# Optimization experiments

Measured on AMD Instinct MI355X. Metric: run time of the kernel, lower is better.

The kernel has to match this reference:

```python
import jax, jax.numpy as jnp
from jax import lax
import numpy as np

# dims
B, T, W, D = 8, 24, 48, 512
H = 8            # n_head
E = D // H       # head dim = 64
DI = 2 * D       # mamba d_inner (expand=2) = 1024
S = 64           # d_state
R = 32           # dt_rank = ceil(512/16)
KC = 4           # mamba depthwise conv kernel
DFF = 2048       # ffn hidden
L = T * W


def setup_inputs() -> dict:
    key = jax.random.key(0)
    ks = jax.random.split(key, 32)
    def g(i, shape, s=0.02):
        return jax.random.normal(ks[i], shape, dtype=jnp.float32) * s
    inp = {
        "x": jax.random.normal(ks[0], (B, T, W, D), dtype=jnp.float32),
        "slf_attn_mask": jnp.zeros((B, L), dtype=bool),
        # attention projections (torch Linear convention: y = x @ W.T + b)
        "Wq": g(1, (D, D)), "bq": jnp.zeros((D,), jnp.float32),
        "Wk": g(2, (D, D)), "bk": jnp.zeros((D,), jnp.float32),
        "Wv": g(3, (D, D)), "bv": jnp.zeros((D,), jnp.float32),
        "Wo": g(4, (D, D)), "bo": jnp.zeros((D,), jnp.float32),
        # mamba params
        "in_proj_w": g(5, (2 * DI, D)),
        "conv_w": g(6, (DI, KC), 0.1),
        "conv_b": jnp.zeros((DI,), jnp.float32),
        "x_proj_w": g(7, (R + 2 * S, DI)),
        "dt_proj_w": g(8, (DI, R), 0.1),
        "dt_proj_b": jnp.full((DI,), -3.0, jnp.float32),  # softplus -> small dt
        "A_log": jnp.broadcast_to(jnp.log(jnp.arange(1, S + 1, dtype=jnp.float32)), (DI, S)).copy(),
        "D_ssm": jnp.ones((DI,), jnp.float32),
        "out_proj_w": g(9, (D, DI)),
        # hybrid LayerNorm
        "ln1_g": jnp.ones((D,), jnp.float32), "ln1_b": jnp.zeros((D,), jnp.float32),
        # FFN (pre-norm)
        "ffn_w1": g(10, (DFF, D)), "ffn_b1": jnp.zeros((DFF,), jnp.float32),
        "ffn_w2": g(11, (D, DFF)), "ffn_b2": jnp.zeros((D,), jnp.float32),
        "ln2_g": jnp.ones((D,), jnp.float32), "ln2_b": jnp.zeros((D,), jnp.float32),
    }
    return inp


def _layernorm(x, g, b, eps):
    m = jnp.mean(x, -1, keepdims=True)
    v = jnp.mean(jnp.square(x - m), -1, keepdims=True)
    return (x - m) * lax.rsqrt(v + eps) * g + b


def _attention(xf, mask, Wq, bq, Wk, bk, Wv, bv, Wo, bo):
    # xf: [B, L, D]; mask: [B, L] bool (True = masked)
    b, l, _ = xf.shape
    q = (xf @ Wq.T + bq).reshape(b, l, H, E)
    k = (xf @ Wk.T + bk).reshape(b, l, H, E)
    v = (xf @ Wv.T + bv).reshape(b, l, H, E)
    scale = 1.0 / jnp.sqrt(jnp.float32(E))
    scores = jnp.einsum('blhe,bshe->bhls', q, k)                 # [B,H,L,L]
    scores = jnp.where(mask[:, None, None, :], -jnp.inf, scores)
    probs = jax.nn.softmax(scale * scores, axis=-1)
    out = jnp.einsum('bhls,bshe->blhe', probs, v).reshape(b, l, D)
    return out @ Wo.T + bo


def _mamba(xf, in_proj_w, conv_w, conv_b, x_proj_w, dt_proj_w, dt_proj_b, A_log, D_ssm, out_proj_w):
    # xf: [B, L, D]
    b, l, _ = xf.shape
    xz = xf @ in_proj_w.T                  # [B,L,2*DI]
    u, z = jnp.split(xz, 2, axis=-1)
    # causal depthwise conv1d, kernel KC
    up = jnp.pad(u, ((0, 0), (KC - 1, 0), (0, 0)))
    uc = conv_b + sum(up[:, k:k + l, :] * conv_w[:, k] for k in range(KC))
    u = jax.nn.silu(uc)                    # [B,L,DI]
    xdbc = u @ x_proj_w.T                  # [B,L,R+2S]
    dt_r, Bm, Cm = jnp.split(xdbc, [R, R + S], axis=-1)
    delta = jax.nn.softplus(dt_r @ dt_proj_w.T + dt_proj_b)   # [B,L,DI]
    A = -jnp.exp(A_log)                    # [DI,S]

    def step(h, xs):
        dt_t, u_t, B_t, C_t = xs           # [B,DI],[B,DI],[B,S],[B,S]
        dA = jnp.exp(dt_t[:, :, None] * A)                       # [B,DI,S]
        h = h * dA + (dt_t * u_t)[:, :, None] * B_t[:, None, :]
        y = jnp.einsum('bds,bs->bd', h, C_t)
        return h, y

    xs = (delta.transpose(1, 0, 2), u.transpose(1, 0, 2),
          Bm.transpose(1, 0, 2), Cm.transpose(1, 0, 2))
    h0 = jnp.zeros((b, DI, S), dtype=xf.dtype)
    _, ys = lax.scan(step, h0, xs)
    y = ys.transpose(1, 0, 2) + u * D_ssm  # [B,L,DI]
    y = y * jax.nn.silu(z)
    return y @ out_proj_w.T


def _forward(x, slf_attn_mask, Wq, bq, Wk, bk, Wv, bv, Wo, bo,
             in_proj_w, conv_w, conv_b, x_proj_w, dt_proj_w, dt_proj_b,
             A_log, D_ssm, out_proj_w, ln1_g, ln1_b,
             ffn_w1, ffn_b1, ffn_w2, ffn_b2, ln2_g, ln2_b):
    b, t, w, d = x.shape
    xf = x.reshape(b, t * w, d)
    x_attn = _attention(xf, slf_attn_mask, Wq, bq, Wk, bk, Wv, bv, Wo, bo)
    x_mamba = _mamba(xf, in_proj_w, conv_w, conv_b, x_proj_w, dt_proj_w,
                     dt_proj_b, A_log, D_ssm, out_proj_w)
    h = xf + x_attn + x_mamba
    h = _layernorm(h, ln1_g, ln1_b, 1e-5)
    # pre-norm FFN with residual
    hn = _layernorm(h, ln2_g, ln2_b, 1e-6)
    ff = jax.nn.gelu(hn @ ffn_w1.T + ffn_b1, approximate=False) @ ffn_w2.T + ffn_b2
    out = h + ff
    return out.reshape(b, t, w, d)


def reference(x, slf_attn_mask, Wq, bq, Wk, bk, Wv, bv, Wo, bo,
              in_proj_w, conv_w, conv_b, x_proj_w, dt_proj_w, dt_proj_b,
              A_log, D_ssm, out_proj_w, ln1_g, ln1_b,
              ffn_w1, ffn_b1, ffn_w2, ffn_b2, ln2_g, ln2_b):
    return _forward(x, slf_attn_mask, Wq, bq, Wk, bk, Wv, bv, Wo, bo,
                    in_proj_w, conv_w, conv_b, x_proj_w, dt_proj_w, dt_proj_b,
                    A_log, D_ssm, out_proj_w, ln1_g, ln1_b,
                    ffn_w1, ffn_b1, ffn_w2, ffn_b2, ln2_g, ln2_b)
```

## Files before the change

### kernel.cpp

```cpp
#include <hip/hip_runtime.h>
#include <hip/hip_bf16.h>
#include <math.h>

#define BB 8
#define DD 512
#define HH 8
#define EE 64
#define DI 1024
#define SS 64
#define RR 32
#define KCONV 4
#define DFF 2048
#define LL 1152
#define ML (BB*LL)
#define XS (RR + 2*SS)
#define ZSTR 2048
#define YSTR 1536

typedef short bf16x8 __attribute__((ext_vector_type(8)));
typedef float f32x4 __attribute__((ext_vector_type(4)));
typedef unsigned short u16x4 __attribute__((ext_vector_type(4)));

#define GLD_LDS(g, l) \
  __builtin_amdgcn_global_load_lds((const __attribute__((address_space(1))) void*)(g), \
                                   (__attribute__((address_space(3))) void*)(l), 16, 0, 0)

__device__ __forceinline__ float bf2f(unsigned short u) {
  return __uint_as_float(((unsigned)u) << 16);
}

template<int IMM>
__device__ __forceinline__ float swz(float x) {
  return __uint_as_float((unsigned)__builtin_amdgcn_ds_swizzle((int)__float_as_uint(x), IMM));
}

__global__ __launch_bounds__(256) void cvt_bf16(
    const float* __restrict__ s, __hip_bfloat16* __restrict__ d, int n)
{
  const int i = (blockIdx.x * 256 + threadIdx.x) * 4;
  if (i + 3 < n) {
    const float4 v = *(const float4*)(s + i);
    __hip_bfloat16 t[4] = {__float2bfloat16(v.x), __float2bfloat16(v.y),
                           __float2bfloat16(v.z), __float2bfloat16(v.w)};
    *(ushort4*)(d + i) = *(const ushort4*)t;
  } else {
    for (int k = i; k < n; ++k) d[k] = __float2bfloat16(s[k]);
  }
}

__global__ __launch_bounds__(256) void cvt_pack(
    const float* __restrict__ s, __hip_bfloat16* __restrict__ d,
    int srclen, int dststride, int dstoff, int total)
{
  const int i = blockIdx.x * 256 + threadIdx.x;
  if (i >= total) return;
  const int r = i / srclen, c = i - r * srclen;
  d[(size_t)r * dststride + dstoff + c] = __float2bfloat16(s[i]);
}

__global__ __launch_bounds__(256) void gemm_mfma(
    const __hip_bfloat16* __restrict__ A, int lda,
    const __hip_bfloat16* __restrict__ W,
    const float* __restrict__ bias,
    const float* __restrict__ res,
    void* __restrict__ Cv, void* __restrict__ Cv2,
    int M, int N, int K, int act, int mode)
{
  __shared__ __align__(16) __hip_bfloat16 As[128 * 32];
  __shared__ __align__(16) __hip_bfloat16 Ws[128 * 32];
  const int tid = threadIdx.x;
  const int wid = tid >> 6, lane = tid & 63;
  const int wr = wid >> 1, wc = wid & 1;
  const int m0 = blockIdx.y << 7, n0 = blockIdx.x << 7;
  const int r1 = tid >> 2;
  const int c1 = (tid & 3) << 3;

  const __hip_bfloat16* ga0 = A + (size_t)(m0 + r1) * lda + c1;
  const __hip_bfloat16* ga1 = A + (size_t)(m0 + 64 + r1) * lda + c1;
  const __hip_bfloat16* gw0 = W + (size_t)(n0 + r1) * K + c1;
  const __hip_bfloat16* gw1 = W + (size_t)(n0 + 64 + r1) * K + c1;
  char* lA0 = (char*)As + wid * 1024;
  char* lA1 = lA0 + 4096;
  char* lW0 = (char*)Ws + wid * 1024;
  char* lW1 = lW0 + 4096;

  f32x4 acc[4][4];
#pragma unroll
  for (int i = 0; i < 4; ++i)
#pragma unroll
    for (int j = 0; j < 4; ++j) acc[i][j] = (f32x4){0.f, 0.f, 0.f, 0.f};

  const int fm = lane & 15;
  const int q8 = (lane >> 4) << 3;

  for (int kt = 0; kt < K; kt += 32) {
    __syncthreads();
    GLD_LDS(ga0, lA0); GLD_LDS(ga1, lA1);
    GLD_LDS(gw0, lW0); GLD_LDS(gw1, lW1);
    ga0 += 32; ga1 += 32; gw0 += 32; gw1 += 32;
    __syncthreads();

    bf16x8 af[4], wf[4];
#pragma unroll
    for (int i = 0; i < 4; ++i)
      af[i] = *(const bf16x8*)((const short*)As + (wr * 64 + i * 16 + fm) * 32 + q8);
#pragma unroll
    for (int j = 0; j < 4; ++j)
      wf[j] = *(const bf16x8*)((const short*)Ws + (wc * 64 + j * 16 + fm) * 32 + q8);
#pragma unroll
    for (int i = 0; i < 4; ++i)
#pragma unroll
      for (int j = 0; j < 4; ++j)
        acc[i][j] = __builtin_amdgcn_mfma_f32_16x16x32_bf16(af[i], wf[j], acc[i][j], 0, 0, 0);
  }

  const int rquad = (lane >> 4) << 2;
#pragma unroll
  for (int j = 0; j < 4; ++j) {
    const int n = n0 + wc * 64 + j * 16 + fm;
    if (n < N) {
      const float bv = bias ? bias[n] : 0.f;
#pragma unroll
      for (int i = 0; i < 4; ++i) {
        const int mb = m0 + wr * 64 + i * 16 + rquad;
#pragma unroll
        for (int r = 0; r < 4; ++r) {
          const int m = mb + r;
          float v = acc[i][j][r] + bv;
          if (act == 1) v = 0.5f * v * (1.f + erff(v * 0.70710678118654752f));
          else if (act == 2) v = fmaxf(v, 0.f) + log1pf(expf(-fabsf(v)));
          if (mode == 3) {
            if (n < 1024) {
              ((__hip_bfloat16*)Cv)[(size_t)m * 1024 + n] = __float2bfloat16(v);
            } else {
              const int e = n - 1024;
              const int bb2 = m / LL;
              const int key = m - bb2 * LL;
              ((__hip_bfloat16*)Cv2)[((size_t)(bb2 * HH + (e >> 6)) * EE + (e & 63)) * LL + key] =
                  __float2bfloat16(v);
            }
          } else {
            const size_t off = (size_t)m * N + n;
            if (res) v += res[off];
            if (mode == 1) ((__hip_bfloat16*)Cv)[off] = __float2bfloat16(v);
            else ((float*)Cv)[off] = v;
          }
        }
      }
    }
  }
}

__global__ __launch_bounds__(256) void conv_silu(
    const __hip_bfloat16* __restrict__ xz, const float* __restrict__ cw,
    const float* __restrict__ cb, __hip_bfloat16* __restrict__ uout)
{
  const size_t idx = (size_t)blockIdx.x * 256 + threadIdx.x;
  if (idx >= (size_t)ML * DI) return;
  const int di = (int)(idx & (DI - 1));
  const int row = (int)(idx >> 10);
  const int t = row % LL;
  float acc = cb[di];
#pragma unroll
  for (int k = 0; k < KCONV; ++k) {
    if (t - (KCONV - 1) + k >= 0)
      acc = fmaf((float)xz[(size_t)(row - (KCONV - 1 - k)) * ZSTR + di],
                 cw[di * KCONV + k], acc);
  }
  uout[idx] = __float2bfloat16(acc / (1.f + __expf(-acc)));
}

#define SLOAD(P_, t0_) { _Pragma("unroll") for (int j = 0; j < 4; ++j) { \
    P_##_dt[j] = bf2f(dp[(size_t)((t0_)+j)*DI]); \
    P_##_u[j]  = bf2f(ubp[(size_t)((t0_)+j)*DI]); \
    P_##_B[j]  = *(const u16x4*)(Bp + (size_t)((t0_)+j)*XS); \
    P_##_C[j]  = *(const u16x4*)(Cp + (size_t)((t0_)+j)*XS); } }

#define SSTEP(P_, j, idx) { \
    const float dtu = P_##_dt[j] * P_##_u[j]; \
    h0 = fmaf(h0, __expf(P_##_dt[j] * Av[0]), dtu * bf2f(P_##_B[j][0])); \
    h1 = fmaf(h1, __expf(P_##_dt[j] * Av[1]), dtu * bf2f(P_##_B[j][1])); \
    h2 = fmaf(h2, __expf(P_##_dt[j] * Av[2]), dtu * bf2f(P_##_B[j][2])); \
    h3 = fmaf(h3, __expf(P_##_dt[j] * Av[3]), dtu * bf2f(P_##_B[j][3])); \
    float part = h0 * bf2f(P_##_C[j][0]); \
    part = fmaf(h1, bf2f(P_##_C[j][1]), part); \
    part = fmaf(h2, bf2f(P_##_C[j][2]), part); \
    part = fmaf(h3, bf2f(P_##_C[j][3]), part); \
    Pp[(idx)] = part; }

#define SCOMP(P_, base_) { \
    SSTEP(P_, 0, (base_)+0) SSTEP(P_, 1, (base_)+1) \
    SSTEP(P_, 2, (base_)+2) SSTEP(P_, 3, (base_)+3) }

__global__ __launch_bounds__(256) void scan_attn(
    const __hip_bfloat16* __restrict__ delta, const __hip_bfloat16* __restrict__ ubf,
    const __hip_bfloat16* __restrict__ xz, const __hip_bfloat16* __restrict__ xdbc,
    const float* __restrict__ A_log, const float* __restrict__ D_ssm,
    const __hip_bfloat16* __restrict__ qk, const __hip_bfloat16* __restrict__ vtg,
    __hip_bfloat16* __restrict__ yattn)
{
  __shared__ __align__(16) __hip_bfloat16 Qs[64][72];
  __shared__ __align__(16) __hip_bfloat16 Ks[64][72];
  __shared__ __align__(16) __hip_bfloat16 Vts[64][72];
  __shared__ __align__(16) __hip_bfloat16 Ps[4][16][72];
  const int tid = threadIdx.x;

  if (blockIdx.x < 512) {
    const int wv = (int)((blockIdx.x * 256 + tid) >> 6);
    const int lane = tid & 63;
    const int c = lane >> 4;
    const int s4 = lane & 15;
    const int g = (wv << 2) + c;
    const int b = g >> 10;
    const int di = g & (DI - 1);
    float Av[4];
#pragma unroll
    for (int kk = 0; kk < 4; ++kk)
      Av[kk] = -__expf(A_log[di * SS + (s4 << 2) + kk]);
    const float Dd = D_ssm[di];
    const size_t rb = (size_t)b * LL;
    const unsigned short* __restrict__ dp = (const unsigned short*)delta + rb * DI + di;
    const unsigned short* __restrict__ ubp = (const unsigned short*)ubf + rb * DI + di;
    const unsigned short* __restrict__ zbp = (const unsigned short*)xz + rb * ZSTR + DI + di;
    const unsigned short* __restrict__ Bp = (const unsigned short*)xdbc + rb * XS + RR + (s4 << 2);
    const unsigned short* __restrict__ Cp = Bp + SS;
    __hip_bfloat16* __restrict__ yp = yattn + rb * YSTR + di;

    float h0 = 0.f, h1 = 0.f, h2 = 0.f, h3 = 0.f;
    float Pp[16];
    float a_dt[4], a_u[4]; u16x4 a_B[4], a_C[4];
    float b_dt[4], b_u[4]; u16x4 b_B[4], b_C[4];
    float c_dt[4], c_u[4]; u16x4 c_B[4], c_C[4];
    float d_dt[4], d_u[4]; u16x4 d_B[4], d_C[4];

    float u_e = bf2f(ubp[(size_t)s4 * DI]);
    float z_e = bf2f(zbp[(size_t)s4 * ZSTR]);

    SLOAD(a, 0) SLOAD(b, 4) SLOAD(c, 8)
    for (int t0 = 0; t0 < LL; t0 += 16) {
      SLOAD(d, t0 + 12)
      SCOMP(a, 0)
      if (t0 + 16 < LL) SLOAD(a, t0 + 16)
      SCOMP(b, 4)
      float u_n = 0.f, z_n = 0.f;
      if (t0 + 16 < LL) {
        u_n = bf2f(ubp[(size_t)(t0 + 16 + s4) * DI]);
        z_n = bf2f(zbp[(size_t)(t0 + 16 + s4) * ZSTR]);
      }
      if (t0 + 20 < LL) SLOAD(b, t0 + 20)
      SCOMP(c, 8)
      if (t0 + 24 < LL) SLOAD(c, t0 + 24)
      SCOMP(d, 12)

#pragma unroll
      for (int k2 = 0; k2 < 8; ++k2) {
        const float mn = (s4 & 1) ? Pp[2*k2+1] : Pp[2*k2];
        const float ot = (s4 & 1) ? Pp[2*k2]   : Pp[2*k2+1];
        Pp[k2] = mn + swz<0x041F>(ot);
      }
#pragma unroll
      for (int k2 = 0; k2 < 4; ++k2) {
        const float mn = (s4 & 2) ? Pp[2*k2+1] : Pp[2*k2];
        const float ot = (s4 & 2) ? Pp[2*k2]   : Pp[2*k2+1];
        Pp[k2] = mn + swz<0x081F>(ot);
      }
#pragma unroll
      for (int k2 = 0; k2 < 2; ++k2) {
        const float mn = (s4 & 4) ? Pp[2*k2+1] : Pp[2*k2];
        const float ot = (s4 & 4) ? Pp[2*k2]   : Pp[2*k2+1];
        Pp[k2] = mn + swz<0x101F>(ot);
      }
      {
        const float mn = (s4 & 8) ? Pp[1] : Pp[0];
        const float ot = (s4 & 8) ? Pp[0] : Pp[1];
        Pp[0] = mn + swz<0x201F>(ot);
      }

      const float yv = (Pp[0] + u_e * Dd) * (z_e / (1.f + __expf(-z_e)));
      yp[(size_t)(t0 + s4) * YSTR] = __float2bfloat16(yv);
      u_e = u_n; z_e = z_n;
    }
    return;
  }

  const int abid = blockIdx.x - 512;
  const int w = tid >> 6, lane = tid & 63;
  const int bh = abid / (LL / 64);
  const int qtile = abid - bh * (LL / 64);
  const int b = bh >> 3, hh = bh & 7;
  const int q0 = qtile << 6;
  const size_t qbase = (size_t)b * LL * 1024 + (size_t)hh * EE;
  const size_t vtbase = (size_t)bh * EE * LL;

  const int srow = tid >> 2, sch = (tid & 3) << 4;
  {
    const __hip_bfloat16* src = qk + qbase + (size_t)(q0 + srow) * 1024 + sch;
    *(uint4*)&Qs[srow][sch]     = *(const uint4*)src;
    *(uint4*)&Qs[srow][sch + 8] = *(const uint4*)(src + 8);
  }
  __syncthreads();

  const int fm = lane & 15;
  const int q8 = (lane >> 4) << 3;
  bf16x8 af0 = *(const bf16x8*)&Qs[w * 16 + fm][q8];
  bf16x8 af1 = *(const bf16x8*)&Qs[w * 16 + fm][32 + q8];

  f32x4 oacc[4];
  float m_i[4], l_i[4];
#pragma unroll
  for (int r = 0; r < 4; ++r) { m_i[r] = -INFINITY; l_i[r] = 0.f; }
#pragma unroll
  for (int j = 0; j < 4; ++j) oacc[j] = (f32x4){0.f, 0.f, 0.f, 0.f};

  for (int kt = 0; kt < LL / 64; ++kt) {
    const int k0 = kt << 6;
    __syncthreads();
    {
      const __hip_bfloat16* ksrc = qk + qbase + 512 + (size_t)(k0 + srow) * 1024 + sch;
      const __hip_bfloat16* vsrc = vtg + vtbase + (size_t)srow * LL + k0 + sch;
      *(uint4*)&Ks[srow][sch]      = *(const uint4*)ksrc;
      *(uint4*)&Ks[srow][sch + 8]  = *(const uint4*)(ksrc + 8);
      *(uint4*)&Vts[srow][sch]     = *(const uint4*)vsrc;
      *(uint4*)&Vts[srow][sch + 8] = *(const uint4*)(vsrc + 8);
    }
    __syncthreads();

    f32x4 sacc[4];
#pragma unroll
    for (int j = 0; j < 4; ++j) sacc[j] = (f32x4){0.f, 0.f, 0.f, 0.f};
#pragma unroll
    for (int j = 0; j < 4; ++j) {
      bf16x8 kf0 = *(const bf16x8*)&Ks[j * 16 + fm][q8];
      bf16x8 kf1 = *(const bf16x8*)&Ks[j * 16 + fm][32 + q8];
      sacc[j] = __builtin_amdgcn_mfma_f32_16x16x32_bf16(af0, kf0, sacc[j], 0, 0, 0);
      sacc[j] = __builtin_amdgcn_mfma_f32_16x16x32_bf16(af1, kf1, sacc[j], 0, 0, 0);
    }

    float alpha[4];
#pragma unroll
    for (int r = 0; r < 4; ++r) {
#pragma unroll
      for (int j = 0; j < 4; ++j) sacc[j][r] *= 0.125f;
      float mt = fmaxf(fmaxf(sacc[0][r], sacc[1][r]), fmaxf(sacc[2][r], sacc[3][r]));
      mt = fmaxf(mt, swz<0x041F>(mt)); mt = fmaxf(mt, swz<0x081F>(mt));
      mt = fmaxf(mt, swz<0x101F>(mt)); mt = fmaxf(mt, swz<0x201F>(mt));
      const float mn = fmaxf(m_i[r], mt);
      alpha[r] = __expf(m_i[r] - mn);
      m_i[r] = mn;
      float p[4], rs = 0.f;
#pragma unroll
      for (int j = 0; j < 4; ++j) { p[j] = __expf(sacc[j][r] - mn); rs += p[j]; }
      rs += swz<0x041F>(rs); rs += swz<0x081F>(rs);
      rs += swz<0x101F>(rs); rs += swz<0x201F>(rs);
      l_i[r] = l_i[r] * alpha[r] + rs;
      const int qrow = ((lane >> 4) << 2) + r;
#pragma unroll
      for (int j = 0; j < 4; ++j)
        Ps[w][qrow][j * 16 + fm] = __float2bfloat16(p[j]);
    }
#pragma unroll
    for (int j = 0; j < 4; ++j)
#pragma unroll
      for (int r = 0; r < 4; ++r) oacc[j][r] *= alpha[r];

    bf16x8 pf0 = *(const bf16x8*)&Ps[w][fm][q8];
    bf16x8 pf1 = *(const bf16x8*)&Ps[w][fm][32 + q8];
#pragma unroll
    for (int j = 0; j < 4; ++j) {
      bf16x8 v0 = *(const bf16x8*)&Vts[j * 16 + fm][q8];
      bf16x8 v1 = *(const bf16x8*)&Vts[j * 16 + fm][32 + q8];
      oacc[j] = __builtin_amdgcn_mfma_f32_16x16x32_bf16(pf0, v0, oacc[j], 0, 0, 0);
      oacc[j] = __builtin_amdgcn_mfma_f32_16x16x32_bf16(pf1, v1, oacc[j], 0, 0, 0);
    }
  }

#pragma unroll
  for (int r = 0; r < 4; ++r) {
    const float inv = 1.f / l_i[r];
    const int qq = q0 + w * 16 + ((lane >> 4) << 2) + r;
#pragma unroll
    for (int j = 0; j < 4; ++j)
      yattn[((size_t)b * LL + qq) * YSTR + 1024 + hh * EE + j * 16 + fm] =
          __float2bfloat16(oacc[j][r] * inv);
  }
}

__device__ __forceinline__ float block_sum512(float val, float* sm)
{
#pragma unroll
  for (int off = 32; off; off >>= 1) val += __shfl_xor(val, off, 64);
  const int wid = threadIdx.x >> 6;
  __syncthreads();
  if ((threadIdx.x & 63) == 0) sm[wid] = val;
  __syncthreads();
  return sm[0] + sm[1] + sm[2] + sm[3];
}

__global__ __launch_bounds__(256) void ln_fused(
    const float* __restrict__ xf, const float* __restrict__ combo,
    const float* __restrict__ g1, const float* __restrict__ b1,
    const float* __restrict__ g2, const float* __restrict__ b2,
    float* __restrict__ hout, __hip_bfloat16* __restrict__ hnout)
{
  __shared__ float sm[4];
  const size_t base = (size_t)blockIdx.x * DD;
  const int t = threadIdx.x;
  const float v0 = xf[base + t] + combo[base + t];
  const float v1 = xf[base + 256 + t] + combo[base + 256 + t];
  const float mean = block_sum512(v0 + v1, sm) * (1.f / DD);
  const float d0 = v0 - mean, d1 = v1 - mean;
  const float var = block_sum512(d0 * d0 + d1 * d1, sm) * (1.f / DD);
  const float rstd = rsqrtf(var + 1e-5f);
  const float h0 = d0 * rstd * g1[t] + b1[t];
  const float h1 = d1 * rstd * g1[t + 256] + b1[t + 256];
  hout[base + t] = h0;
  hout[base + 256 + t] = h1;
  const float mean2 = block_sum512(h0 + h1, sm) * (1.f / DD);
  const float e0 = h0 - mean2, e1 = h1 - mean2;
  const float var2 = block_sum512(e0 * e0 + e1 * e1, sm) * (1.f / DD);
  const float rstd2 = rsqrtf(var2 + 1e-6f);
  hnout[base + t] = __float2bfloat16(e0 * rstd2 * g2[t] + b2[t]);
  hnout[base + 256 + t] = __float2bfloat16(e1 * rstd2 * g2[t + 256] + b2[t + 256]);
}

extern "C" void kernel_launch(void* const* d_in, const int* in_sizes, int n_in,
                              void* d_out, int out_size, void* d_ws, size_t ws_size,
                              hipStream_t stream)
{
  const float* x         = (const float*)d_in[0];
  const float* Wq        = (const float*)d_in[2];
  const float* bq        = (const float*)d_in[3];
  const float* Wk        = (const float*)d_in[4];
  const float* bk        = (const float*)d_in[5];
  const float* Wv        = (const float*)d_in[6];
  const float* bv        = (const float*)d_in[7];
  const float* Wo        = (const float*)d_in[8];
  const float* bo        = (const float*)d_in[9];
  const float* in_proj_w = (const float*)d_in[10];
  const float* conv_w    = (const float*)d_in[11];
  const float* conv_b    = (const float*)d_in[12];
  const float* x_proj_w  = (const float*)d_in[13];
  const float* dt_proj_w = (const float*)d_in[14];
  const float* dt_proj_b = (const float*)d_in[15];
  const float* A_log     = (const float*)d_in[16];
  const float* D_ssm     = (const float*)d_in[17];
  const float* out_proj_w= (const float*)d_in[18];
  const float* ln1_g     = (const float*)d_in[19];
  const float* ln1_b     = (const float*)d_in[20];
  const float* ffn_w1    = (const float*)d_in[21];
  const float* ffn_b1    = (const float*)d_in[22];
  const float* ffn_w2    = (const float*)d_in[23];
  const float* ffn_b2    = (const float*)d_in[24];
  const float* ln2_g     = (const float*)d_in[25];
  const float* ln2_b     = (const float*)d_in[26];
  float* out = (float*)d_out;

  float* ws = (float*)d_ws;
  const size_t OF_XBF = 2506752;
  const size_t OF_XZ  = OF_XBF + 2359296;
  const size_t OF_UBF = OF_XZ + 9437184;
  const size_t OF_XD  = OF_UBF + 4718592;
  const size_t OF_DF  = OF_XD + 737280;
  const size_t OF_QKV = OF_DF + 4718592;
  const size_t OF_YA  = OF_QKV + 7077888;
  const size_t OF_QB  = OF_YA + 7077888;

  __hip_bfloat16* wbf     = (__hip_bfloat16*)ws;
  __hip_bfloat16* xbf     = (__hip_bfloat16*)(ws + OF_XBF);
  __hip_bfloat16* hnbf    = (__hip_bfloat16*)(ws + OF_XBF);
  __hip_bfloat16* xz      = (__hip_bfloat16*)(ws + OF_XZ);
  __hip_bfloat16* ubf     = (__hip_bfloat16*)(ws + OF_UBF);
  float*          combo   = ws + OF_UBF;
  __hip_bfloat16* xdbc_bf = (__hip_bfloat16*)(ws + OF_XD);
  __hip_bfloat16* deltab  = (__hip_bfloat16*)(ws + OF_DF);
  __hip_bfloat16* ffbf    = (__hip_bfloat16*)(ws + OF_DF);
  __hip_bfloat16* qkbuf   = (__hip_bfloat16*)(ws + OF_QKV);
  __hip_bfloat16* vtbf    = (__hip_bfloat16*)(ws + OF_QKV + 4718592);
  __hip_bfloat16* yattn   = (__hip_bfloat16*)(ws + OF_YA);
  float*          hbuf    = ws + OF_YA;
  float*          qkvbias = ws + OF_QB;

  const size_t w_inproj = 0;
  const size_t w_xproj  = 1048576;
  const size_t w_dt     = 1310720;
  const size_t w_cat    = 1343488;
  const size_t w_q      = 2129920;
  const size_t w_f1     = 2916352;
  const size_t w_f2     = 3964928;

  const dim3 thr(256);
#define CVT(src, dst, n) cvt_bf16<<<dim3(((n)/4 + 255)/256), thr, 0, stream>>>(src, dst, n)
#define GEMM(Abf, lda_, Woff, Bptr, Rptr, Cptr, C2ptr, N_, K_, act_, md_) \
  gemm_mfma<<<dim3((N_ + 127)/128, ML/128), thr, 0, stream>>>( \
      Abf, lda_, wbf + (Woff), Bptr, Rptr, (void*)(Cptr), (void*)(C2ptr), ML, N_, K_, act_, md_)

  hipMemsetAsync((void*)(wbf + w_xproj + (size_t)160 * 1024), 0, (size_t)96 * 1024 * 2, stream);
  CVT(in_proj_w, wbf + w_inproj, 1048576);
  CVT(x_proj_w,  wbf + w_xproj,  163840);
  CVT(dt_proj_w, wbf + w_dt,     32768);
  cvt_pack<<<dim3((524288 + 255)/256), thr, 0, stream>>>(
      out_proj_w, wbf + w_cat, 1024, 1536, 0,    524288);
  cvt_pack<<<dim3((262144 + 255)/256), thr, 0, stream>>>(
      Wo,         wbf + w_cat, 512,  1536, 1024, 262144);
  CVT(Wq,        wbf + w_q,           262144);
  CVT(Wk,        wbf + w_q + 262144,  262144);
  CVT(Wv,        wbf + w_q + 524288,  262144);
  CVT(ffn_w1,    wbf + w_f1,    1048576);
  CVT(ffn_w2,    wbf + w_f2,    1048576);
  CVT(x,         xbf,           ML * DD);
  hipMemcpyAsync(qkvbias,        bq, 512 * sizeof(float), hipMemcpyDeviceToDevice, stream);
  hipMemcpyAsync(qkvbias + 512,  bk, 512 * sizeof(float), hipMemcpyDeviceToDevice, stream);
  hipMemcpyAsync(qkvbias + 1024, bv, 512 * sizeof(float), hipMemcpyDeviceToDevice, stream);

  GEMM(xbf, DD, w_inproj, nullptr, nullptr, xz, nullptr, 2 * DI, DD, 0, 1);
  conv_silu<<<dim3((ML * DI) / 256), thr, 0, stream>>>(xz, conv_w, conv_b, ubf);
  GEMM(ubf, DI, w_xproj, nullptr, nullptr, xdbc_bf, nullptr, XS, DI, 0, 1);
  GEMM(xdbc_bf, XS, w_dt, dt_proj_b, nullptr, deltab, nullptr, DI, RR, 2, 1);

  GEMM(xbf, DD, w_q, qkvbias, nullptr, qkbuf, vtbf, 3 * DD, DD, 0, 3);

  scan_attn<<<dim3(512 + BB * HH * (LL / 64)), thr, 0, stream>>>(
      deltab, ubf, xz, xdbc_bf, A_log, D_ssm, qkbuf, vtbf, yattn);

  GEMM(yattn, YSTR, w_cat, bo, nullptr, combo, nullptr, DD, YSTR, 0, 0);

  ln_fused<<<dim3(ML), thr, 0, stream>>>(x, combo, ln1_g, ln1_b,
                                         ln2_g, ln2_b, hbuf, hnbf);

  GEMM(hnbf, DD, w_f1, ffn_b1, nullptr, ffbf, nullptr, DFF, DD, 1, 1);
  GEMM(ffbf, DFF, w_f2, ffn_b2, hbuf, out, nullptr, DD, DFF, 0, 0);
#undef GEMM
#undef CVT
}
```

Baseline: 1.036 ms.

## Split fused scan/attention kernel and spread SSM state across full wavefront

Splits the combined scan+attention kernel into two separate launches, one for attention and one for the selective scan. The scan now gives each wavefront one (batch, channel) pair with one state element per lane (64 lanes), where before each lane handled 4 states. This cuts per-thread serial work and registers, which allows 8 blocks per CU and 4x more scan waves. It also precomputes dt*u at load time and uses exp2f with a log2e-scaled A. In exchange the kernels no longer overlap within a single launch, and each step needs a longer cross-lane reduction (extra swizzle and shuffle), with redundant B/C/dt loads per lane.

```diff
diff --git a/kernel.cpp b/kernel.cpp
--- a/kernel.cpp
+++ b/kernel.cpp
@@ -19,7 +19,6 @@
 
 typedef short bf16x8 __attribute__((ext_vector_type(8)));
 typedef float f32x4 __attribute__((ext_vector_type(4)));
-typedef unsigned short u16x4 __attribute__((ext_vector_type(4)));
 
 #define GLD_LDS(g, l) \
   __builtin_amdgcn_global_load_lds((const __attribute__((address_space(1))) void*)(g), \
@@ -171,124 +170,112 @@
 }
 
 #define SLOAD(P_, t0_) { _Pragma("unroll") for (int j = 0; j < 4; ++j) { \
-    P_##_dt[j] = bf2f(dp[(size_t)((t0_)+j)*DI]); \
-    P_##_u[j]  = bf2f(ubp[(size_t)((t0_)+j)*DI]); \
-    P_##_B[j]  = *(const u16x4*)(Bp + (size_t)((t0_)+j)*XS); \
-    P_##_C[j]  = *(const u16x4*)(Cp + (size_t)((t0_)+j)*XS); } }
+    const float dtv = bf2f(dp[(size_t)((t0_)+j)*DI]); \
+    P_##_dt[j] = dtv; \
+    P_##_du[j] = dtv * bf2f(ubp[(size_t)((t0_)+j)*DI]); \
+    P_##_B[j]  = Bp[(size_t)((t0_)+j)*XS]; \
+    P_##_C[j]  = Cp[(size_t)((t0_)+j)*XS]; } }
 
 #define SSTEP(P_, j, idx) { \
-    const float dtu = P_##_dt[j] * P_##_u[j]; \
-    h0 = fmaf(h0, __expf(P_##_dt[j] * Av[0]), dtu * bf2f(P_##_B[j][0])); \
-    h1 = fmaf(h1, __expf(P_##_dt[j] * Av[1]), dtu * bf2f(P_##_B[j][1])); \
-    h2 = fmaf(h2, __expf(P_##_dt[j] * Av[2]), dtu * bf2f(P_##_B[j][2])); \
-    h3 = fmaf(h3, __expf(P_##_dt[j] * Av[3]), dtu * bf2f(P_##_B[j][3])); \
-    float part = h0 * bf2f(P_##_C[j][0]); \
-    part = fmaf(h1, bf2f(P_##_C[j][1]), part); \
-    part = fmaf(h2, bf2f(P_##_C[j][2]), part); \
-    part = fmaf(h3, bf2f(P_##_C[j][3]), part); \
-    Pp[(idx)] = part; }
+    const float dA = exp2f(P_##_dt[j] * Av); \
+    h = fmaf(h, dA, P_##_du[j] * bf2f(P_##_B[j])); \
+    Pp[(idx)] = h * bf2f(P_##_C[j]); }
 
 #define SCOMP(P_, base_) { \
     SSTEP(P_, 0, (base_)+0) SSTEP(P_, 1, (base_)+1) \
     SSTEP(P_, 2, (base_)+2) SSTEP(P_, 3, (base_)+3) }
 
-__global__ __launch_bounds__(256) void scan_attn(
+__global__ __launch_bounds__(256, 8) void scan_kernel(
     const __hip_bfloat16* __restrict__ delta, const __hip_bfloat16* __restrict__ ubf,
     const __hip_bfloat16* __restrict__ xz, const __hip_bfloat16* __restrict__ xdbc,
     const float* __restrict__ A_log, const float* __restrict__ D_ssm,
-    const __hip_bfloat16* __restrict__ qk, const __hip_bfloat16* __restrict__ vtg,
     __hip_bfloat16* __restrict__ yattn)
+{
+  const int wv = (int)((blockIdx.x * 256 + threadIdx.x) >> 6);
+  const int lane = threadIdx.x & 63;
+  const int b = wv >> 10;
+  const int di = wv & (DI - 1);
+  const float Av = -__expf(A_log[di * SS + lane]) * 1.4426950408889634f;
+  const float Dd = D_ssm[di];
+  const size_t rb = (size_t)b * LL;
+  const unsigned short* __restrict__ dp  = (const unsigned short*)delta + rb * DI + di;
+  const unsigned short* __restrict__ ubp = (const unsigned short*)ubf + rb * DI + di;
+  const unsigned short* __restrict__ zbp = (const unsigned short*)xz + rb * ZSTR + DI + di;
+  const unsigned short* __restrict__ Bp  = (const unsigned short*)xdbc + rb * XS + RR + lane;
+  const unsigned short* __restrict__ Cp  = Bp + SS;
+  __hip_bfloat16* __restrict__ yp = yattn + rb * YSTR + di;
+
+  const int l15 = lane & 15;
+  float h = 0.f;
+  float Pp[16];
+  float a_dt[4], a_du[4]; unsigned short a_B[4], a_C[4];
+  float b_dt[4], b_du[4]; unsigned short b_B[4], b_C[4];
+
+  float u_e = bf2f(ubp[(size_t)l15 * DI]);
+  float z_e = bf2f(zbp[(size_t)l15 * ZSTR]);
+
+  SLOAD(a, 0)
+  for (int t0 = 0; t0 < LL; t0 += 16) {
+    SLOAD(b, t0 + 4)
+    SCOMP(a, 0)
+    SLOAD(a, t0 + 8)
+    SCOMP(b, 4)
+    float u_n = 0.f, z_n = 0.f;
+    if (t0 + 16 < LL) {
+      u_n = bf2f(ubp[(size_t)(t0 + 16 + l15) * DI]);
+      z_n = bf2f(zbp[(size_t)(t0 + 16 + l15) * ZSTR]);
+    }
+    SLOAD(b, t0 + 12)
+    SCOMP(a, 8)
+    if (t0 + 16 < LL) SLOAD(a, t0 + 16)
+    SCOMP(b, 12)
+
+#pragma unroll
+    for (int k2 = 0; k2 < 8; ++k2) {
+      const float mn = (lane & 1) ? Pp[2*k2+1] : Pp[2*k2];
+      const float ot = (lane & 1) ? Pp[2*k2]   : Pp[2*k2+1];
+      Pp[k2] = mn + swz<0x041F>(ot);
+    }
+#pragma unroll
+    for (int k2 = 0; k2 < 4; ++k2) {
+      const float mn = (lane & 2) ? Pp[2*k2+1] : Pp[2*k2];
+      const float ot = (lane & 2) ? Pp[2*k2]   : Pp[2*k2+1];
+      Pp[k2] = mn + swz<0x081F>(ot);
+    }
+#pragma unroll
+    for (int k2 = 0; k2 < 2; ++k2) {
+      const float mn = (lane & 4) ? Pp[2*k2+1] : Pp[2*k2];
+      const float ot = (lane & 4) ? Pp[2*k2]   : Pp[2*k2+1];
+      Pp[k2] = mn + swz<0x101F>(ot);
+    }
+    {
+      const float mn = (lane & 8) ? Pp[1] : Pp[0];
+      const float ot = (lane & 8) ? Pp[0] : Pp[1];
+      Pp[0] = mn + swz<0x201F>(ot);
+    }
+    Pp[0] += swz<0x401F>(Pp[0]);
+    Pp[0] += __shfl_xor(Pp[0], 32, 64);
+
+    const float yv = (Pp[0] + u_e * Dd) * (z_e / (1.f + __expf(-z_e)));
+    if (lane < 16)
+      yp[(size_t)(t0 + lane) * YSTR] = __float2bfloat16(yv);
+    u_e = u_n; z_e = z_n;
+  }
+}
+
+__global__ __launch_bounds__(256) void attn_mfma(
+    const __hip_bfloat16* __restrict__ qk,
+    const __hip_bfloat16* __restrict__ vtg, __hip_bfloat16* __restrict__ yattn)
 {
   __shared__ __align__(16) __hip_bfloat16 Qs[64][72];
   __shared__ __align__(16) __hip_bfloat16 Ks[64][72];
   __shared__ __align__(16) __hip_bfloat16 Vts[64][72];
   __shared__ __align__(16) __hip_bfloat16 Ps[4][16][72];
   const int tid = threadIdx.x;
-
-  if (blockIdx.x < 512) {
-    const int wv = (int)((blockIdx.x * 256 + tid) >> 6);
-    const int lane = tid & 63;
-    const int c = lane >> 4;
-    const int s4 = lane & 15;
-    const int g = (wv << 2) + c;
-    const int b = g >> 10;
-    const int di = g & (DI - 1);
-    float Av[4];
-#pragma unroll
-    for (int kk = 0; kk < 4; ++kk)
-      Av[kk] = -__expf(A_log[di * SS + (s4 << 2) + kk]);
-    const float Dd = D_ssm[di];
-    const size_t rb = (size_t)b * LL;
-    const unsigned short* __restrict__ dp = (const unsigned short*)delta + rb * DI + di;
-    const unsigned short* __restrict__ ubp = (const unsigned short*)ubf + rb * DI + di;
-    const unsigned short* __restrict__ zbp = (const unsigned short*)xz + rb * ZSTR + DI + di;
-    const unsigned short* __restrict__ Bp = (const unsigned short*)xdbc + rb * XS + RR + (s4 << 2);
-    const unsigned short* __restrict__ Cp = Bp + SS;
-    __hip_bfloat16* __restrict__ yp = yattn + rb * YSTR + di;
-
-    float h0 = 0.f, h1 = 0.f, h2 = 0.f, h3 = 0.f;
-    float Pp[16];
-    float a_dt[4], a_u[4]; u16x4 a_B[4], a_C[4];
-    float b_dt[4], b_u[4]; u16x4 b_B[4], b_C[4];
-    float c_dt[4], c_u[4]; u16x4 c_B[4], c_C[4];
-    float d_dt[4], d_u[4]; u16x4 d_B[4], d_C[4];
-
-    float u_e = bf2f(ubp[(size_t)s4 * DI]);
-    float z_e = bf2f(zbp[(size_t)s4 * ZSTR]);
-
-    SLOAD(a, 0) SLOAD(b, 4) SLOAD(c, 8)
-    for (int t0 = 0; t0 < LL; t0 += 16) {
-      SLOAD(d, t0 + 12)
-      SCOMP(a, 0)
-      if (t0 + 16 < LL) SLOAD(a, t0 + 16)
-      SCOMP(b, 4)
-      float u_n = 0.f, z_n = 0.f;
-      if (t0 + 16 < LL) {
-        u_n = bf2f(ubp[(size_t)(t0 + 16 + s4) * DI]);
-        z_n = bf2f(zbp[(size_t)(t0 + 16 + s4) * ZSTR]);
-      }
-      if (t0 + 20 < LL) SLOAD(b, t0 + 20)
-      SCOMP(c, 8)
-      if (t0 + 24 < LL) SLOAD(c, t0 + 24)
-      SCOMP(d, 12)
-
-#pragma unroll
-      for (int k2 = 0; k2 < 8; ++k2) {
-        const float mn = (s4 & 1) ? Pp[2*k2+1] : Pp[2*k2];
-        const float ot = (s4 & 1) ? Pp[2*k2]   : Pp[2*k2+1];
-        Pp[k2] = mn + swz<0x041F>(ot);
-      }
-#pragma unroll
-      for (int k2 = 0; k2 < 4; ++k2) {
-        const float mn = (s4 & 2) ? Pp[2*k2+1] : Pp[2*k2];
-        const float ot = (s4 & 2) ? Pp[2*k2]   : Pp[2*k2+1];
-        Pp[k2] = mn + swz<0x081F>(ot);
-      }
-#pragma unroll
-      for (int k2 = 0; k2 < 2; ++k2) {
-        const float mn = (s4 & 4) ? Pp[2*k2+1] : Pp[2*k2];
-        const float ot = (s4 & 4) ? Pp[2*k2]   : Pp[2*k2+1];
-        Pp[k2] = mn + swz<0x101F>(ot);
-      }
-      {
-        const float mn = (s4 & 8) ? Pp[1] : Pp[0];
-        const float ot = (s4 & 8) ? Pp[0] : Pp[1];
-        Pp[0] = mn + swz<0x201F>(ot);
-      }
-
-      const float yv = (Pp[0] + u_e * Dd) * (z_e / (1.f + __expf(-z_e)));
-      yp[(size_t)(t0 + s4) * YSTR] = __float2bfloat16(yv);
-      u_e = u_n; z_e = z_n;
-    }
-    return;
-  }
-
-  const int abid = blockIdx.x - 512;
   const int w = tid >> 6, lane = tid & 63;
-  const int bh = abid / (LL / 64);
-  const int qtile = abid - bh * (LL / 64);
+  const int bh = blockIdx.y;
   const int b = bh >> 3, hh = bh & 7;
-  const int q0 = qtile << 6;
+  const int q0 = blockIdx.x << 6;
   const size_t qbase = (size_t)b * LL * 1024 + (size_t)hh * EE;
   const size_t vtbase = (size_t)bh * EE * LL;
 
@@ -518,9 +505,10 @@
   GEMM(xdbc_bf, XS, w_dt, dt_proj_b, nullptr, deltab, nullptr, DI, RR, 2, 1);
 
   GEMM(xbf, DD, w_q, qkvbias, nullptr, qkbuf, vtbf, 3 * DD, DD, 0, 3);
-
-  scan_attn<<<dim3(512 + BB * HH * (LL / 64)), thr, 0, stream>>>(
-      deltab, ubf, xz, xdbc_bf, A_log, D_ssm, qkbuf, vtbf, yattn);
+  attn_mfma<<<dim3(LL / 64, BB * HH), thr, 0, stream>>>(qkbuf, vtbf, yattn);
+
+  scan_kernel<<<dim3(2048), thr, 0, stream>>>(
+      deltab, ubf, xz, xdbc_bf, A_log, D_ssm, yattn);
 
   GEMM(yattn, YSTR, w_cat, bo, nullptr, combo, nullptr, DD, YSTR, 0, 0);
 
```

Result: slower. 3.007 ms (+190.2%).
